# Kernel optimization log

Hardware: AMD Instinct MI355X
Metric: run time of the kernel (lower is better)

Reference implementation:

```python
import jax, jax.numpy as jnp
import numpy as np

B, IN, L0, L1, H, NT = 4096, 1024, 2048, 1024, 128, 512
T = 0.1          # temperature (nonzero -> soft indicator)
EPS = 1e-5       # BatchNorm eps


def setup_inputs() -> dict:
    key = jax.random.key(0)
    ks = jax.random.split(key, 12)

    def he(k, fin, fout):
        return jax.random.normal(k, (fin, fout), jnp.float32) * (2.0 / fin) ** 0.5

    dec_raw = jax.random.uniform(ks[10], (H, IN), jnp.float32)
    # mimics dec_weight_scaled = rand(h, in) / row_sum
    dec_w = dec_raw / dec_raw.sum(axis=1, keepdims=True)

    return {
        "x": jax.random.normal(ks[0], (B, IN), jnp.float32),
        # uniform noise driving the exponential reparameterized draws
        "u": jax.random.uniform(ks[1], (B, NT, H), jnp.float32, minval=1e-7, maxval=1.0),
        "enc1_w": he(ks[2], IN, L0), "enc1_b": jnp.zeros(L0, jnp.float32),
        "bn1_g": jnp.ones(L0, jnp.float32), "bn1_b": jnp.zeros(L0, jnp.float32),
        "enc2_w": he(ks[3], L0, L1), "enc2_b": jnp.zeros(L1, jnp.float32),
        "bn2_g": jnp.ones(L1, jnp.float32), "bn2_b": jnp.zeros(L1, jnp.float32),
        "enc3_w": he(ks[4], L1, H), "enc3_b": jnp.zeros(H, jnp.float32),
        "bn3_g": jnp.ones(H, jnp.float32), "bn3_b": jnp.zeros(H, jnp.float32),
        "inp_lamb_w": jax.random.normal(ks[5], (H, H), jnp.float32) * (1.0 / H) ** 0.5,
        "inp_lamb_b": jnp.zeros(H, jnp.float32),
        "dec_w": dec_w,
    }


def _bn(x, g, b):
    # BatchNorm1d in training mode: batch statistics, biased variance
    m = x.mean(axis=0)
    v = ((x - m) ** 2).mean(axis=0)
    return g * (x - m) / jnp.sqrt(v + EPS) + b


def reference(x, u, enc1_w, enc1_b, bn1_g, bn1_b, enc2_w, enc2_b, bn2_g, bn2_b,
              enc3_w, enc3_b, bn3_g, bn3_b, inp_lamb_w, inp_lamb_b, dec_w):
    # ---- encoder ----
    h = jax.nn.relu(_bn(x @ enc1_w + enc1_b, bn1_g, bn1_b))
    h = jax.nn.relu(_bn(h @ enc2_w + enc2_b, bn2_g, bn2_b))
    h = jax.nn.relu(_bn(h @ enc3_w + enc3_b, bn3_g, bn3_b))
    lamb = jnp.abs(h @ inp_lamb_w + inp_lamb_b)              # [B,H]

    # ---- decoder matrix normalization ----
    diag = jax.lax.stop_gradient(jnp.abs(dec_w.sum(axis=1)))  # [H], detached
    decode = jnp.abs(dec_w) / diag[:, None]                   # [H,IN]
    rate = jnp.clip(lamb * diag, 1e-10, 1e7)                  # [B,H]

    # ---- Poisson rsample via cumulative exponential inter-arrival times ----
    # Exponential(rate) draws: -log(u)/rate ; cumsum over trials; soft indicator
    e = -jnp.log(u) / rate[:, None, :]                        # [B,NT,H]
    times = jnp.cumsum(e, axis=1)                             # [B,NT,H]
    indicator = jax.nn.sigmoid((1.0 - times) / T)             # soft (t != 0)
    samples = indicator.sum(axis=1)                           # [B,H]

    x_rec = samples @ decode                                  # [B,IN]
    return (x_rec, samples, rate, decode)
```

## Files before the change

kernel.cpp:

```cpp
#include <hip/hip_runtime.h>
#include <stdint.h>


typedef __attribute__((ext_vector_type(8))) __bf16 bf16x8;
typedef __attribute__((ext_vector_type(4))) float f32x4;
typedef unsigned short ushort_t;

__device__ __forceinline__ unsigned short f2bf(float f) {
  unsigned int u = __float_as_uint(f);
  unsigned int r = (u + 0x7fffu + ((u >> 16) & 1u)) >> 16;
  return (unsigned short)r;
}
__device__ __forceinline__ float bf2f(unsigned short h) {
  return __uint_as_float(((unsigned int)h) << 16);
}

__device__ __forceinline__ void gll16(const void* g, void* l) {
  __builtin_amdgcn_global_load_lds(
      (const __attribute__((address_space(1))) unsigned int*)g,
      (__attribute__((address_space(3))) unsigned int*)l, 16, 0, 0);
}

__global__ void kconvert_split4(const float4* __restrict__ in, ushort4* __restrict__ hi,
                                ushort4* __restrict__ lo, int n4) {
  int i = blockIdx.x * blockDim.x + threadIdx.x;
  if (i < n4) {
    float4 v = in[i];
    ushort4 h, l;
    h.x = f2bf(v.x); l.x = f2bf(v.x - bf2f(h.x));
    h.y = f2bf(v.y); l.y = f2bf(v.y - bf2f(h.y));
    h.z = f2bf(v.z); l.z = f2bf(v.z - bf2f(h.z));
    h.w = f2bf(v.w); l.w = f2bf(v.w - bf2f(h.w));
    hi[i] = h; lo[i] = l;
  }
}

__global__ void ktranspose_split(const float* __restrict__ in, unsigned short* __restrict__ ohi,
                                 unsigned short* __restrict__ olo, int R, int C) {
  __shared__ unsigned short th[32][33];
  __shared__ unsigned short tl[32][33];
  int c0 = blockIdx.x * 32, r0 = blockIdx.y * 32;
  int tx = threadIdx.x & 31, ty = threadIdx.x >> 5;
#pragma unroll
  for (int i = 0; i < 32; i += 8) {
    float v = in[(size_t)(r0 + ty + i) * C + c0 + tx];
    unsigned short h = f2bf(v);
    th[ty + i][tx] = h;
    tl[ty + i][tx] = f2bf(v - bf2f(h));
  }
  __syncthreads();
#pragma unroll
  for (int i = 0; i < 32; i += 8) {
    ohi[(size_t)(c0 + ty + i) * R + r0 + tx] = th[tx][ty + i];
    olo[(size_t)(c0 + ty + i) * R + r0 + tx] = tl[tx][ty + i];
  }
}

__global__ __launch_bounds__(256) void kgemm3p(
    const unsigned short* __restrict__ Ah, const unsigned short* __restrict__ Al,
    const unsigned short* __restrict__ Bh, const unsigned short* __restrict__ Bl,
    const float* __restrict__ bias, float* __restrict__ C, int N, int K, int kLen,
    float* __restrict__ bnps, float* __restrict__ bnpq, const float* __restrict__ diag) {
  __shared__ unsigned short As[2][4096];
  __shared__ unsigned short Bs[2][4096];
  __shared__ float sred[2][2][128];
  int tid = threadIdx.x;
  int lane = tid & 63;
  int wave = tid >> 6;
  int wm = wave >> 1, wn = wave & 1;
  int rowBase = blockIdx.x * 128;
  int colBase = blockIdx.y * 128;
  int kOff = blockIdx.z * kLen;
  C += (size_t)blockIdx.z * gridDim.x * 128 * N;

  f32x4 acc[4][4];
#pragma unroll
  for (int i = 0; i < 4; i++)
#pragma unroll
    for (int j = 0; j < 4; j++) acc[i][j] = (f32x4){0.f, 0.f, 0.f, 0.f};

  int r4 = tid >> 2;
  int kc = (tid & 3) * 8;
  int lr = lane & 15;
  int lk = (lane >> 4) * 8;

  const unsigned short* Ah0 = Ah + (size_t)(rowBase + r4) * K + kOff + kc;
  const unsigned short* Al0 = Al + (size_t)(rowBase + r4) * K + kOff + kc;
  const unsigned short* Bh0 = Bh + (size_t)(colBase + r4) * K + kOff + kc;
  const unsigned short* Bl0 = Bl + (size_t)(colBase + r4) * K + kOff + kc;
  size_t rstep = (size_t)64 * K;
  char* AsD = (char*)As + tid * 16;
  char* BsD = (char*)Bs + tid * 16;

  gll16(Ah0, AsD);        gll16(Ah0 + rstep, AsD + 4096);
  gll16(Al0, AsD + 8192); gll16(Al0 + rstep, AsD + 12288);
  gll16(Bh0, BsD);        gll16(Bh0 + rstep, BsD + 4096);
  gll16(Bl0, BsD + 8192); gll16(Bl0 + rstep, BsD + 12288);
  __syncthreads();

  int nk = kLen >> 5;
  for (int kt = 0; kt < nk; ++kt) {
    bf16x8 ah[4], al[4], bh[4], bl[4];
#pragma unroll
    for (int mi = 0; mi < 4; mi++) {
      ah[mi] = *(const bf16x8*)&As[0][(wm * 64 + mi * 16 + lr) * 32 + lk];
      al[mi] = *(const bf16x8*)&As[1][(wm * 64 + mi * 16 + lr) * 32 + lk];
      bh[mi] = *(const bf16x8*)&Bs[0][(wn * 64 + mi * 16 + lr) * 32 + lk];
      bl[mi] = *(const bf16x8*)&Bs[1][(wn * 64 + mi * 16 + lr) * 32 + lk];
    }
    __syncthreads();

    if (kt + 1 < nk) {
      int k0 = (kt + 1) << 5;
      gll16(Ah0 + k0, AsD);        gll16(Ah0 + k0 + rstep, AsD + 4096);
      gll16(Al0 + k0, AsD + 8192); gll16(Al0 + k0 + rstep, AsD + 12288);
      gll16(Bh0 + k0, BsD);        gll16(Bh0 + k0 + rstep, BsD + 4096);
      gll16(Bl0 + k0, BsD + 8192); gll16(Bl0 + k0 + rstep, BsD + 12288);
    }

#pragma unroll
    for (int mi = 0; mi < 4; mi++)
#pragma unroll
      for (int ni = 0; ni < 4; ni++) {
        acc[mi][ni] = __builtin_amdgcn_mfma_f32_16x16x32_bf16(ah[mi], bh[ni], acc[mi][ni], 0, 0, 0);
        acc[mi][ni] = __builtin_amdgcn_mfma_f32_16x16x32_bf16(ah[mi], bl[ni], acc[mi][ni], 0, 0, 0);
        acc[mi][ni] = __builtin_amdgcn_mfma_f32_16x16x32_bf16(al[mi], bh[ni], acc[mi][ni], 0, 0, 0);
      }
    __syncthreads();
  }

  int lg = lane >> 4;
  if (diag) {
#pragma unroll
    for (int mi = 0; mi < 4; mi++)
#pragma unroll
      for (int ni = 0; ni < 4; ni++) {
        int col = colBase + wn * 64 + ni * 16 + lr;
        float bv = bias ? bias[col] : 0.0f;
        float dg = diag[col];
#pragma unroll
        for (int j = 0; j < 4; j++) {
          int row = rowBase + wm * 64 + mi * 16 + lg * 4 + j;
          float r = fabsf(acc[mi][ni][j] + bv) * dg;
          C[(size_t)row * N + col] = fminf(fmaxf(r, 1e-10f), 1e7f);
        }
      }
  } else {
    float s[4] = {0.f, 0.f, 0.f, 0.f}, q[4] = {0.f, 0.f, 0.f, 0.f};
#pragma unroll
    for (int mi = 0; mi < 4; mi++)
#pragma unroll
      for (int ni = 0; ni < 4; ni++) {
        int col = colBase + wn * 64 + ni * 16 + lr;
        float bv = bias ? bias[col] : 0.0f;
#pragma unroll
        for (int j = 0; j < 4; j++) {
          int row = rowBase + wm * 64 + mi * 16 + lg * 4 + j;
          float v = acc[mi][ni][j] + bv;
          C[(size_t)row * N + col] = v;
          s[ni] += v;
          q[ni] += v * v;
        }
      }
    if (bnps) {
#pragma unroll
      for (int ni = 0; ni < 4; ni++) {
        s[ni] += __shfl_xor(s[ni], 16); s[ni] += __shfl_xor(s[ni], 32);
        q[ni] += __shfl_xor(q[ni], 16); q[ni] += __shfl_xor(q[ni], 32);
      }
      if (lg == 0) {
#pragma unroll
        for (int ni = 0; ni < 4; ni++) {
          sred[wm][0][wn * 64 + ni * 16 + lr] = s[ni];
          sred[wm][1][wn * 64 + ni * 16 + lr] = q[ni];
        }
      }
      __syncthreads();
      if (tid < 128) {
        bnps[(size_t)blockIdx.x * N + colBase + tid] = sred[0][0][tid] + sred[1][0][tid];
        bnpq[(size_t)blockIdx.x * N + colBase + tid] = sred[0][1][tid] + sred[1][1][tid];
      }
    }
  }
}

__global__ __launch_bounds__(256) void kgemm(
    const unsigned short* __restrict__ A, const unsigned short* __restrict__ BT,
    float* __restrict__ C, int N, int K) {
  __shared__ unsigned short As[4096];
  __shared__ unsigned short Bs[4096];
  int tid = threadIdx.x;
  int lane = tid & 63;
  int wave = tid >> 6;
  int wm = wave >> 1, wn = wave & 1;
  int rowBase = blockIdx.x * 128;
  int colBase = blockIdx.y * 128;

  f32x4 acc[4][4];
#pragma unroll
  for (int i = 0; i < 4; i++)
#pragma unroll
    for (int j = 0; j < 4; j++) acc[i][j] = (f32x4){0.f, 0.f, 0.f, 0.f};

  int r4 = tid >> 2;
  int kc = (tid & 3) * 8;
  int lr = lane & 15;
  int lk = (lane >> 4) * 8;

  const unsigned short* A0 = A + (size_t)(rowBase + r4) * K + kc;
  const unsigned short* B0 = BT + (size_t)(colBase + r4) * K + kc;
  size_t rstep = (size_t)64 * K;
  char* AsD = (char*)As + tid * 16;
  char* BsD = (char*)Bs + tid * 16;

  gll16(A0, AsD); gll16(A0 + rstep, AsD + 4096);
  gll16(B0, BsD); gll16(B0 + rstep, BsD + 4096);
  __syncthreads();

  int nk = K >> 5;
  for (int kt = 0; kt < nk; ++kt) {
    bf16x8 af[4], bfr[4];
#pragma unroll
    for (int mi = 0; mi < 4; mi++) {
      af[mi] = *(const bf16x8*)&As[(wm * 64 + mi * 16 + lr) * 32 + lk];
      bfr[mi] = *(const bf16x8*)&Bs[(wn * 64 + mi * 16 + lr) * 32 + lk];
    }
    __syncthreads();
    if (kt + 1 < nk) {
      int k0 = (kt + 1) << 5;
      gll16(A0 + k0, AsD); gll16(A0 + k0 + rstep, AsD + 4096);
      gll16(B0 + k0, BsD); gll16(B0 + k0 + rstep, BsD + 4096);
    }
#pragma unroll
    for (int mi = 0; mi < 4; mi++)
#pragma unroll
      for (int ni = 0; ni < 4; ni++)
        acc[mi][ni] = __builtin_amdgcn_mfma_f32_16x16x32_bf16(af[mi], bfr[ni], acc[mi][ni], 0, 0, 0);
    __syncthreads();
  }

  int lg = lane >> 4;
#pragma unroll
  for (int mi = 0; mi < 4; mi++)
#pragma unroll
    for (int ni = 0; ni < 4; ni++) {
      int col = colBase + wn * 64 + ni * 16 + lr;
#pragma unroll
      for (int j = 0; j < 4; j++) {
        int row = rowBase + wm * 64 + mi * 16 + lg * 4 + j;
        C[(size_t)row * N + col] = acc[mi][ni][j];
      }
    }
}

__global__ void kbn_partial(const float* __restrict__ y, float* __restrict__ ps,
                            float* __restrict__ pq, int N) {
  int c = blockIdx.x * blockDim.x + threadIdx.x;
  int r0 = blockIdx.y * 128;
  float s = 0.f, q = 0.f;
  for (int r = r0; r < r0 + 128; ++r) {
    float v = y[(size_t)r * N + c];
    s += v;
    q += v * v;
  }
  ps[blockIdx.y * N + c] = s;
  pq[blockIdx.y * N + c] = q;
}

__global__ void kbn_final(const float* __restrict__ ps, const float* __restrict__ pq,
                          const float* __restrict__ g, const float* __restrict__ b,
                          float* __restrict__ scale, float* __restrict__ shift, int N,
                          int stripes) {
  int c = blockIdx.x * blockDim.x + threadIdx.x;
  if (c >= N) return;
  float s = 0.f, q = 0.f;
  for (int i = 0; i < stripes; ++i) {
    s += ps[i * N + c];
    q += pq[i * N + c];
  }
  float m = s * (1.0f / 4096.0f);
  float var = q * (1.0f / 4096.0f) - m * m;
  float sc = g[c] * rsqrtf(var + 1e-5f);
  scale[c] = sc;
  shift[c] = b[c] - m * sc;
}

__global__ void kbn_apply_split4(const float4* __restrict__ y, const float* __restrict__ scale,
                                 const float* __restrict__ shift, ushort4* __restrict__ hhi,
                                 ushort4* __restrict__ hlo, int mask) {
  int i = blockIdx.x * blockDim.x + threadIdx.x;
  int c0 = (i << 2) & mask;
  float4 v = y[i];
  ushort4 h, l;
  float t;
  t = v.x * scale[c0] + shift[c0];         t = t > 0.f ? t : 0.f; h.x = f2bf(t); l.x = f2bf(t - bf2f(h.x));
  t = v.y * scale[c0 + 1] + shift[c0 + 1]; t = t > 0.f ? t : 0.f; h.y = f2bf(t); l.y = f2bf(t - bf2f(h.y));
  t = v.z * scale[c0 + 2] + shift[c0 + 2]; t = t > 0.f ? t : 0.f; h.z = f2bf(t); l.z = f2bf(t - bf2f(h.z));
  t = v.w * scale[c0 + 3] + shift[c0 + 3]; t = t > 0.f ? t : 0.f; h.w = f2bf(t); l.w = f2bf(t - bf2f(h.w));
  hhi[i] = h;
  hlo[i] = l;
}

__global__ void kcombine(const float4* __restrict__ Cp, const float* __restrict__ bias,
                         float4* __restrict__ y, int n4, int splitStride4, int splits, int mask) {
  int i = blockIdx.x * blockDim.x + threadIdx.x;
  if (i >= n4) return;
  int c0 = (i << 2) & mask;
  float4 a = Cp[i];
  for (int z = 1; z < splits; ++z) {
    float4 b = Cp[(size_t)z * splitStride4 + i];
    a.x += b.x; a.y += b.y; a.z += b.z; a.w += b.w;
  }
  a.x += bias[c0]; a.y += bias[c0 + 1]; a.z += bias[c0 + 2]; a.w += bias[c0 + 3];
  y[i] = a;
}

__global__ void kdec(const float* __restrict__ dec_w, float* __restrict__ decode,
                     unsigned short* __restrict__ decT, float* __restrict__ diag) {
  int h = blockIdx.x, tx = threadIdx.x;
  __shared__ float red[256];
  float s = 0.f;
  for (int i = tx; i < 1024; i += 256) s += dec_w[h * 1024 + i];
  red[tx] = s;
  __syncthreads();
  for (int k = 128; k > 0; k >>= 1) {
    if (tx < k) red[tx] += red[tx + k];
    __syncthreads();
  }
  float d = fabsf(red[0]);
  if (tx == 0) diag[h] = d;
  float inv = 1.0f / d;
  for (int i = tx; i < 1024; i += 256) {
    float v = fabsf(dec_w[h * 1024 + i]) * inv;
    decode[h * 1024 + i] = v;
    decT[i * 128 + h] = f2bf(v);
  }
}

__global__ __launch_bounds__(256) void kpoisson(const float* __restrict__ u,
                                                const float* __restrict__ rate,
                                                float* __restrict__ samples,
                                                unsigned short* __restrict__ sb) {
  int tid = blockIdx.x * 256 + threadIdx.x;
  int h = tid & 127;
  int b = tid >> 7;
  float r = rate[tid];
  float inv = 1.0f / r;
  const float* up = u + (size_t)b * (512 * 128) + h;
  float t = 0.f, s = 0.f;
  for (int nt = 0; nt < 512; ++nt) {
    float uv = up[(size_t)nt * 128];
    t += (-__logf(uv)) * inv;
    float z = (t - 1.0f) * 10.0f;
    s += __frcp_rn(1.0f + __expf(z));
    if (t > 4.0f) break;
  }
  samples[tid] = s;
  sb[tid] = f2bf(s);
}

extern "C" void kernel_launch(void* const* d_in, const int* in_sizes, int n_in,
                              void* d_out, int out_size, void* d_ws, size_t ws_size,
                              hipStream_t stream) {
  const float* x = (const float*)d_in[0];
  const float* u = (const float*)d_in[1];
  const float* w1 = (const float*)d_in[2];
  const float* b1 = (const float*)d_in[3];
  const float* g1 = (const float*)d_in[4];
  const float* bb1 = (const float*)d_in[5];
  const float* w2 = (const float*)d_in[6];
  const float* b2 = (const float*)d_in[7];
  const float* g2 = (const float*)d_in[8];
  const float* bb2 = (const float*)d_in[9];
  const float* w3 = (const float*)d_in[10];
  const float* b3 = (const float*)d_in[11];
  const float* g3 = (const float*)d_in[12];
  const float* bb3 = (const float*)d_in[13];
  const float* w4 = (const float*)d_in[14];
  const float* b4 = (const float*)d_in[15];
  const float* dw = (const float*)d_in[16];

  float* out = (float*)d_out;
  float* out_xrec = out;
  float* out_samp = out + 4194304;
  float* out_rate = out + 4718592;
  float* out_dec = out + 5242880;

  char* w = (char*)d_ws;
  unsigned short* xhi = (unsigned short*)w;  w += 8388608;
  unsigned short* xlo = (unsigned short*)w;  w += 8388608;
  unsigned short* w1th = (unsigned short*)w; w += 4194304;
  unsigned short* w1tl = (unsigned short*)w; w += 4194304;
  unsigned short* w2th = (unsigned short*)w; w += 4194304;
  unsigned short* w2tl = (unsigned short*)w; w += 4194304;
  unsigned short* w3th = (unsigned short*)w; w += 262144;
  unsigned short* w3tl = (unsigned short*)w; w += 262144;
  unsigned short* w4th = (unsigned short*)w; w += 32768;
  unsigned short* w4tl = (unsigned short*)w; w += 32768;
  float* y = (float*)w;             w += 33554432;
  unsigned short* h1h = (unsigned short*)w; w += 16777216;
  unsigned short* h1l = (unsigned short*)w; w += 16777216;
  unsigned short* h2h = (unsigned short*)w; w += 8388608;
  unsigned short* h2l = (unsigned short*)w; w += 8388608;
  unsigned short* h3h = (unsigned short*)w; w += 1048576;
  unsigned short* h3l = (unsigned short*)w; w += 1048576;
  float* y3 = (float*)w;            w += 2097152;
  float* Cp = (float*)w;            w += 8388608;
  unsigned short* sb = (unsigned short*)w; w += 1048576;
  unsigned short* dct = (unsigned short*)w; w += 262144;
  float* diag = (float*)w;          w += 1024;
  float* ps = (float*)w;            w += 262144;
  float* pq = (float*)w;            w += 262144;
  float* scale = (float*)w;         w += 8192;
  float* shift = (float*)w;         w += 8192;

  kconvert_split4<<<4096, 256, 0, stream>>>((const float4*)x, (ushort4*)xhi, (ushort4*)xlo, 1048576);
  ktranspose_split<<<dim3(64, 32), 256, 0, stream>>>(w1, w1th, w1tl, 1024, 2048);
  ktranspose_split<<<dim3(32, 64), 256, 0, stream>>>(w2, w2th, w2tl, 2048, 1024);
  ktranspose_split<<<dim3(4, 32), 256, 0, stream>>>(w3, w3th, w3tl, 1024, 128);
  ktranspose_split<<<dim3(4, 4), 256, 0, stream>>>(w4, w4th, w4tl, 128, 128);
  kdec<<<128, 256, 0, stream>>>(dw, out_dec, dct, diag);

  kgemm3p<<<dim3(32, 16), 256, 0, stream>>>(xhi, xlo, w1th, w1tl, b1, y, 2048, 1024, 1024,
                                            ps, pq, nullptr);
  kbn_final<<<8, 256, 0, stream>>>(ps, pq, g1, bb1, scale, shift, 2048, 32);
  kbn_apply_split4<<<8192, 256, 0, stream>>>((const float4*)y, scale, shift, (ushort4*)h1h,
                                             (ushort4*)h1l, 2047);

  kgemm3p<<<dim3(32, 8), 256, 0, stream>>>(h1h, h1l, w2th, w2tl, b2, y, 1024, 2048, 2048,
                                           ps, pq, nullptr);
  kbn_final<<<4, 256, 0, stream>>>(ps, pq, g2, bb2, scale, shift, 1024, 32);
  kbn_apply_split4<<<4096, 256, 0, stream>>>((const float4*)y, scale, shift, (ushort4*)h2h,
                                             (ushort4*)h2l, 1023);

  kgemm3p<<<dim3(32, 1, 4), 256, 0, stream>>>(h2h, h2l, w3th, w3tl, nullptr, Cp, 128, 1024, 256,
                                              nullptr, nullptr, nullptr);
  kcombine<<<512, 256, 0, stream>>>((const float4*)Cp, b3, (float4*)y3, 131072, 131072, 4, 127);
  kbn_partial<<<dim3(1, 32), 128, 0, stream>>>(y3, ps, pq, 128);
  kbn_final<<<1, 128, 0, stream>>>(ps, pq, g3, bb3, scale, shift, 128, 32);
  kbn_apply_split4<<<512, 256, 0, stream>>>((const float4*)y3, scale, shift, (ushort4*)h3h,
                                            (ushort4*)h3l, 127);

  kgemm3p<<<dim3(32, 1), 256, 0, stream>>>(h3h, h3l, w4th, w4tl, b4, out_rate, 128, 128, 128,
                                           nullptr, nullptr, diag);

  kpoisson<<<2048, 256, 0, stream>>>(u, out_rate, out_samp, sb);

  kgemm<<<dim3(32, 8), 256, 0, stream>>>(sb, dct, out_xrec, 1024, 128);
}
```

Baseline: 275.0 us.

## Add 256-row GEMM tile, split-K layer 2, fuse combine with BN stats

Adds a 256x128 tiled three-pass bf16 GEMM kernel used for the first two encoder layers, doubling A-tile reuse of B fragments per block. Layer 2 now uses split-K by 2 into a larger partial buffer, and a new kernel sums the splits, adds bias and computes BatchNorm partial sums in one pass. Layer 3 goes to split-K by 8 with the same fused combine/stats, replacing a separate combine and partial-stat kernel. The cost is more register pressure and fewer blocks per GEMM, plus extra partial-buffer traffic for the split-K layers.

```diff
diff --git a/kernel.cpp b/kernel.cpp
--- a/kernel.cpp
+++ b/kernel.cpp
@@ -4,7 +4,6 @@
 
 typedef __attribute__((ext_vector_type(8))) __bf16 bf16x8;
 typedef __attribute__((ext_vector_type(4))) float f32x4;
-typedef unsigned short ushort_t;
 
 __device__ __forceinline__ unsigned short f2bf(float f) {
   unsigned int u = __float_as_uint(f);
@@ -56,14 +55,137 @@
   }
 }
 
+__global__ __launch_bounds__(256, 2) void kgemm3p256(
+    const unsigned short* __restrict__ Ah, const unsigned short* __restrict__ Al,
+    const unsigned short* __restrict__ Bh, const unsigned short* __restrict__ Bl,
+    const float* __restrict__ bias, float* __restrict__ C, int N, int K, int kLen,
+    float* __restrict__ bnps, float* __restrict__ bnpq) {
+  __shared__ unsigned short As[2][8192];
+  __shared__ unsigned short Bs[2][4096];
+  __shared__ float sred[2][2][128];
+  int tid = threadIdx.x;
+  int lane = tid & 63;
+  int wave = tid >> 6;
+  int wm = wave >> 1, wn = wave & 1;
+  int rowBase = blockIdx.x * 256;
+  int colBase = blockIdx.y * 128;
+  int kOff = blockIdx.z * kLen;
+  C += (size_t)blockIdx.z * gridDim.x * 256 * N;
+
+  f32x4 acc[8][4];
+#pragma unroll
+  for (int i = 0; i < 8; i++)
+#pragma unroll
+    for (int j = 0; j < 4; j++) acc[i][j] = (f32x4){0.f, 0.f, 0.f, 0.f};
+
+  int r4 = tid >> 2;
+  int kc = (tid & 3) * 8;
+  int lr = lane & 15;
+  int lk = (lane >> 4) * 8;
+
+  const unsigned short* Ah0 = Ah + (size_t)(rowBase + r4) * K + kOff + kc;
+  const unsigned short* Al0 = Al + (size_t)(rowBase + r4) * K + kOff + kc;
+  const unsigned short* Bh0 = Bh + (size_t)(colBase + r4) * K + kOff + kc;
+  const unsigned short* Bl0 = Bl + (size_t)(colBase + r4) * K + kOff + kc;
+  size_t rstep = (size_t)64 * K;
+  char* AsD = (char*)As + tid * 16;
+  char* BsD = (char*)Bs + tid * 16;
+
+  auto STAGE = [&](int k0) {
+    gll16(Ah0 + k0, AsD);
+    gll16(Ah0 + k0 + rstep, AsD + 4096);
+    gll16(Ah0 + k0 + 2 * rstep, AsD + 8192);
+    gll16(Ah0 + k0 + 3 * rstep, AsD + 12288);
+    gll16(Al0 + k0, AsD + 16384);
+    gll16(Al0 + k0 + rstep, AsD + 20480);
+    gll16(Al0 + k0 + 2 * rstep, AsD + 24576);
+    gll16(Al0 + k0 + 3 * rstep, AsD + 28672);
+    gll16(Bh0 + k0, BsD);
+    gll16(Bh0 + k0 + rstep, BsD + 4096);
+    gll16(Bl0 + k0, BsD + 8192);
+    gll16(Bl0 + k0 + rstep, BsD + 12288);
+  };
+
+  STAGE(0);
+  __syncthreads();
+
+  int nk = kLen >> 5;
+  for (int kt = 0; kt < nk; ++kt) {
+    bf16x8 ah[8], al[8], bh[4], bl[4];
+#pragma unroll
+    for (int mi = 0; mi < 8; mi++) {
+      ah[mi] = *(const bf16x8*)&As[0][(wm * 128 + mi * 16 + lr) * 32 + lk];
+      al[mi] = *(const bf16x8*)&As[1][(wm * 128 + mi * 16 + lr) * 32 + lk];
+    }
+#pragma unroll
+    for (int ni = 0; ni < 4; ni++) {
+      bh[ni] = *(const bf16x8*)&Bs[0][(wn * 64 + ni * 16 + lr) * 32 + lk];
+      bl[ni] = *(const bf16x8*)&Bs[1][(wn * 64 + ni * 16 + lr) * 32 + lk];
+    }
+    __syncthreads();
+
+    if (kt + 1 < nk) STAGE((kt + 1) << 5);
+
+#pragma unroll
+    for (int mi = 0; mi < 8; mi++)
+#pragma unroll
+      for (int ni = 0; ni < 4; ni++) {
+        acc[mi][ni] = __builtin_amdgcn_mfma_f32_16x16x32_bf16(ah[mi], bh[ni], acc[mi][ni], 0, 0, 0);
+        acc[mi][ni] = __builtin_amdgcn_mfma_f32_16x16x32_bf16(ah[mi], bl[ni], acc[mi][ni], 0, 0, 0);
+      }
+#pragma unroll
+    for (int mi = 0; mi < 8; mi++)
+#pragma unroll
+      for (int ni = 0; ni < 4; ni++)
+        acc[mi][ni] = __builtin_amdgcn_mfma_f32_16x16x32_bf16(al[mi], bh[ni], acc[mi][ni], 0, 0, 0);
+    __syncthreads();
+  }
+
+  int lg = lane >> 4;
+  float s[4] = {0.f, 0.f, 0.f, 0.f}, q[4] = {0.f, 0.f, 0.f, 0.f};
+#pragma unroll
+  for (int mi = 0; mi < 8; mi++)
+#pragma unroll
+    for (int ni = 0; ni < 4; ni++) {
+      int col = colBase + wn * 64 + ni * 16 + lr;
+      float bv = bias ? bias[col] : 0.0f;
+#pragma unroll
+      for (int j = 0; j < 4; j++) {
+        int row = rowBase + wm * 128 + mi * 16 + lg * 4 + j;
+        float v = acc[mi][ni][j] + bv;
+        C[(size_t)row * N + col] = v;
+        s[ni] += v;
+        q[ni] += v * v;
+      }
+    }
+  if (bnps) {
+#pragma unroll
+    for (int ni = 0; ni < 4; ni++) {
+      s[ni] += __shfl_xor(s[ni], 16); s[ni] += __shfl_xor(s[ni], 32);
+      q[ni] += __shfl_xor(q[ni], 16); q[ni] += __shfl_xor(q[ni], 32);
+    }
+    if (lg == 0) {
+#pragma unroll
+      for (int ni = 0; ni < 4; ni++) {
+        sred[wm][0][wn * 64 + ni * 16 + lr] = s[ni];
+        sred[wm][1][wn * 64 + ni * 16 + lr] = q[ni];
+      }
+    }
+    __syncthreads();
+    if (tid < 128) {
+      bnps[(size_t)blockIdx.x * N + colBase + tid] = sred[0][0][tid] + sred[1][0][tid];
+      bnpq[(size_t)blockIdx.x * N + colBase + tid] = sred[0][1][tid] + sred[1][1][tid];
+    }
+  }
+}
+
 __global__ __launch_bounds__(256) void kgemm3p(
     const unsigned short* __restrict__ Ah, const unsigned short* __restrict__ Al,
     const unsigned short* __restrict__ Bh, const unsigned short* __restrict__ Bl,
     const float* __restrict__ bias, float* __restrict__ C, int N, int K, int kLen,
-    float* __restrict__ bnps, float* __restrict__ bnpq, const float* __restrict__ diag) {
+    const float* __restrict__ diag) {
   __shared__ unsigned short As[2][4096];
   __shared__ unsigned short Bs[2][4096];
-  __shared__ float sred[2][2][128];
   int tid = threadIdx.x;
   int lane = tid & 63;
   int wave = tid >> 6;
@@ -109,7 +231,6 @@
       bl[mi] = *(const bf16x8*)&Bs[1][(wn * 64 + mi * 16 + lr) * 32 + lk];
     }
     __syncthreads();
-
     if (kt + 1 < nk) {
       int k0 = (kt + 1) << 5;
       gll16(Ah0 + k0, AsD);        gll16(Ah0 + k0 + rstep, AsD + 4096);
@@ -117,7 +238,6 @@
       gll16(Bh0 + k0, BsD);        gll16(Bh0 + k0 + rstep, BsD + 4096);
       gll16(Bl0 + k0, BsD + 8192); gll16(Bl0 + k0 + rstep, BsD + 12288);
     }
-
 #pragma unroll
     for (int mi = 0; mi < 4; mi++)
 #pragma unroll
@@ -130,58 +250,21 @@
   }
 
   int lg = lane >> 4;
-  if (diag) {
-#pragma unroll
-    for (int mi = 0; mi < 4; mi++)
-#pragma unroll
-      for (int ni = 0; ni < 4; ni++) {
-        int col = colBase + wn * 64 + ni * 16 + lr;
-        float bv = bias ? bias[col] : 0.0f;
-        float dg = diag[col];
-#pragma unroll
-        for (int j = 0; j < 4; j++) {
-          int row = rowBase + wm * 64 + mi * 16 + lg * 4 + j;
-          float r = fabsf(acc[mi][ni][j] + bv) * dg;
-          C[(size_t)row * N + col] = fminf(fmaxf(r, 1e-10f), 1e7f);
-        }
+#pragma unroll
+  for (int mi = 0; mi < 4; mi++)
+#pragma unroll
+    for (int ni = 0; ni < 4; ni++) {
+      int col = colBase + wn * 64 + ni * 16 + lr;
+      float bv = bias ? bias[col] : 0.0f;
+      float dg = diag ? diag[col] : 0.0f;
+#pragma unroll
+      for (int j = 0; j < 4; j++) {
+        int row = rowBase + wm * 64 + mi * 16 + lg * 4 + j;
+        float v = acc[mi][ni][j] + bv;
+        if (diag) v = fminf(fmaxf(fabsf(v) * dg, 1e-10f), 1e7f);
+        C[(size_t)row * N + col] = v;
       }
-  } else {
-    float s[4] = {0.f, 0.f, 0.f, 0.f}, q[4] = {0.f, 0.f, 0.f, 0.f};
-#pragma unroll
-    for (int mi = 0; mi < 4; mi++)
-#pragma unroll
-      for (int ni = 0; ni < 4; ni++) {
-        int col = colBase + wn * 64 + ni * 16 + lr;
-        float bv = bias ? bias[col] : 0.0f;
-#pragma unroll
-        for (int j = 0; j < 4; j++) {
-          int row = rowBase + wm * 64 + mi * 16 + lg * 4 + j;
-          float v = acc[mi][ni][j] + bv;
-          C[(size_t)row * N + col] = v;
-          s[ni] += v;
-          q[ni] += v * v;
-        }
-      }
-    if (bnps) {
-#pragma unroll
-      for (int ni = 0; ni < 4; ni++) {
-        s[ni] += __shfl_xor(s[ni], 16); s[ni] += __shfl_xor(s[ni], 32);
-        q[ni] += __shfl_xor(q[ni], 16); q[ni] += __shfl_xor(q[ni], 32);
-      }
-      if (lg == 0) {
-#pragma unroll
-        for (int ni = 0; ni < 4; ni++) {
-          sred[wm][0][wn * 64 + ni * 16 + lr] = s[ni];
-          sred[wm][1][wn * 64 + ni * 16 + lr] = q[ni];
-        }
-      }
-      __syncthreads();
-      if (tid < 128) {
-        bnps[(size_t)blockIdx.x * N + colBase + tid] = sred[0][0][tid] + sred[1][0][tid];
-        bnpq[(size_t)blockIdx.x * N + colBase + tid] = sred[0][1][tid] + sred[1][1][tid];
-      }
-    }
-  }
+    }
 }
 
 __global__ __launch_bounds__(256) void kgemm(
@@ -253,13 +336,17 @@
     }
 }
 
-__global__ void kbn_partial(const float* __restrict__ y, float* __restrict__ ps,
-                            float* __restrict__ pq, int N) {
-  int c = blockIdx.x * blockDim.x + threadIdx.x;
+__global__ void kcombine_bn(const float* __restrict__ Cp, const float* __restrict__ bias,
+                            float* __restrict__ y, float* __restrict__ ps, float* __restrict__ pq,
+                            int N, int splits, int splitStride) {
+  int c = blockIdx.x * 128 + threadIdx.x;
   int r0 = blockIdx.y * 128;
+  float bv = bias[c];
   float s = 0.f, q = 0.f;
   for (int r = r0; r < r0 + 128; ++r) {
-    float v = y[(size_t)r * N + c];
+    float v = bv;
+    for (int z = 0; z < splits; ++z) v += Cp[(size_t)z * splitStride + (size_t)r * N + c];
+    y[(size_t)r * N + c] = v;
     s += v;
     q += v * v;
   }
@@ -299,20 +386,6 @@
   t = v.w * scale[c0 + 3] + shift[c0 + 3]; t = t > 0.f ? t : 0.f; h.w = f2bf(t); l.w = f2bf(t - bf2f(h.w));
   hhi[i] = h;
   hlo[i] = l;
-}
-
-__global__ void kcombine(const float4* __restrict__ Cp, const float* __restrict__ bias,
-                         float4* __restrict__ y, int n4, int splitStride4, int splits, int mask) {
-  int i = blockIdx.x * blockDim.x + threadIdx.x;
-  if (i >= n4) return;
-  int c0 = (i << 2) & mask;
-  float4 a = Cp[i];
-  for (int z = 1; z < splits; ++z) {
-    float4 b = Cp[(size_t)z * splitStride4 + i];
-    a.x += b.x; a.y += b.y; a.z += b.z; a.w += b.w;
-  }
-  a.x += bias[c0]; a.y += bias[c0 + 1]; a.z += bias[c0 + 2]; a.w += bias[c0 + 3];
-  y[i] = a;
 }
 
 __global__ void kdec(const float* __restrict__ dec_w, float* __restrict__ decode,
@@ -405,7 +478,7 @@
   unsigned short* h3h = (unsigned short*)w; w += 1048576;
   unsigned short* h3l = (unsigned short*)w; w += 1048576;
   float* y3 = (float*)w;            w += 2097152;
-  float* Cp = (float*)w;            w += 8388608;
+  float* Cp = (float*)w;            w += 33554432;
   unsigned short* sb = (unsigned short*)w; w += 1048576;
   unsigned short* dct = (unsigned short*)w; w += 262144;
   float* diag = (float*)w;          w += 1024;
@@ -421,28 +494,28 @@
   ktranspose_split<<<dim3(4, 4), 256, 0, stream>>>(w4, w4th, w4tl, 128, 128);
   kdec<<<128, 256, 0, stream>>>(dw, out_dec, dct, diag);
 
-  kgemm3p<<<dim3(32, 16), 256, 0, stream>>>(xhi, xlo, w1th, w1tl, b1, y, 2048, 1024, 1024,
-                                            ps, pq, nullptr);
-  kbn_final<<<8, 256, 0, stream>>>(ps, pq, g1, bb1, scale, shift, 2048, 32);
+  kgemm3p256<<<dim3(16, 16), 256, 0, stream>>>(xhi, xlo, w1th, w1tl, b1, y, 2048, 1024, 1024,
+                                               ps, pq);
+  kbn_final<<<8, 256, 0, stream>>>(ps, pq, g1, bb1, scale, shift, 2048, 16);
   kbn_apply_split4<<<8192, 256, 0, stream>>>((const float4*)y, scale, shift, (ushort4*)h1h,
                                              (ushort4*)h1l, 2047);
 
-  kgemm3p<<<dim3(32, 8), 256, 0, stream>>>(h1h, h1l, w2th, w2tl, b2, y, 1024, 2048, 2048,
-                                           ps, pq, nullptr);
+  kgemm3p256<<<dim3(16, 8, 2), 256, 0, stream>>>(h1h, h1l, w2th, w2tl, nullptr, Cp, 1024, 2048,
+                                                 1024, nullptr, nullptr);
+  kcombine_bn<<<dim3(8, 32), 128, 0, stream>>>(Cp, b2, y, ps, pq, 1024, 2, 4194304);
   kbn_final<<<4, 256, 0, stream>>>(ps, pq, g2, bb2, scale, shift, 1024, 32);
   kbn_apply_split4<<<4096, 256, 0, stream>>>((const float4*)y, scale, shift, (ushort4*)h2h,
                                              (ushort4*)h2l, 1023);
 
-  kgemm3p<<<dim3(32, 1, 4), 256, 0, stream>>>(h2h, h2l, w3th, w3tl, nullptr, Cp, 128, 1024, 256,
-                                              nullptr, nullptr, nullptr);
-  kcombine<<<512, 256, 0, stream>>>((const float4*)Cp, b3, (float4*)y3, 131072, 131072, 4, 127);
-  kbn_partial<<<dim3(1, 32), 128, 0, stream>>>(y3, ps, pq, 128);
+  kgemm3p<<<dim3(32, 1, 8), 256, 0, stream>>>(h2h, h2l, w3th, w3tl, nullptr, Cp, 128, 1024, 128,
+                                              nullptr);
+  kcombine_bn<<<dim3(1, 32), 128, 0, stream>>>(Cp, b3, y3, ps, pq, 128, 8, 524288);
   kbn_final<<<1, 128, 0, stream>>>(ps, pq, g3, bb3, scale, shift, 128, 32);
   kbn_apply_split4<<<512, 256, 0, stream>>>((const float4*)y3, scale, shift, (ushort4*)h3h,
                                             (ushort4*)h3l, 127);
 
   kgemm3p<<<dim3(32, 1), 256, 0, stream>>>(h3h, h3l, w4th, w4tl, b4, out_rate, 128, 128, 128,
-                                           nullptr, nullptr, diag);
+                                           diag);
 
   kpoisson<<<2048, 256, 0, stream>>>(u, out_rate, out_samp, sb);
 
```

New measurement: 599.6 us. 2.18x slower.

## Split-K the second and third encoder GEMMs and fuse combine with BN stats

Applied to the files above, without the earlier changes.

The second encoder GEMM moves from a 256-block launch to split-K over 2 slices (512 blocks) writing partial sums. A new kernel sums the partials, adds the bias and accumulates BatchNorm partial statistics in the same pass. The third GEMM goes from 4 to 8 K-splits, and the separate combine and bn_partial kernels are merged. This trades extra global traffic for the fp32 partial buffers (a larger Cp workspace) against better occupancy on the many-CU GPU, and the column-per-thread combine loop is scalar and strided by row.

```diff
diff --git a/kernel.cpp b/kernel.cpp
--- a/kernel.cpp
+++ b/kernel.cpp
@@ -4,7 +4,6 @@
 
 typedef __attribute__((ext_vector_type(8))) __bf16 bf16x8;
 typedef __attribute__((ext_vector_type(4))) float f32x4;
-typedef unsigned short ushort_t;
 
 __device__ __forceinline__ unsigned short f2bf(float f) {
   unsigned int u = __float_as_uint(f);
@@ -253,13 +252,17 @@
     }
 }
 
-__global__ void kbn_partial(const float* __restrict__ y, float* __restrict__ ps,
-                            float* __restrict__ pq, int N) {
-  int c = blockIdx.x * blockDim.x + threadIdx.x;
+__global__ void kcombine_bn(const float* __restrict__ Cp, const float* __restrict__ bias,
+                            float* __restrict__ y, float* __restrict__ ps, float* __restrict__ pq,
+                            int N, int splits, int splitStride) {
+  int c = blockIdx.x * 128 + threadIdx.x;
   int r0 = blockIdx.y * 128;
+  float bv = bias[c];
   float s = 0.f, q = 0.f;
   for (int r = r0; r < r0 + 128; ++r) {
-    float v = y[(size_t)r * N + c];
+    float v = bv;
+    for (int z = 0; z < splits; ++z) v += Cp[(size_t)z * splitStride + (size_t)r * N + c];
+    y[(size_t)r * N + c] = v;
     s += v;
     q += v * v;
   }
@@ -299,20 +302,6 @@
   t = v.w * scale[c0 + 3] + shift[c0 + 3]; t = t > 0.f ? t : 0.f; h.w = f2bf(t); l.w = f2bf(t - bf2f(h.w));
   hhi[i] = h;
   hlo[i] = l;
-}
-
-__global__ void kcombine(const float4* __restrict__ Cp, const float* __restrict__ bias,
-                         float4* __restrict__ y, int n4, int splitStride4, int splits, int mask) {
-  int i = blockIdx.x * blockDim.x + threadIdx.x;
-  if (i >= n4) return;
-  int c0 = (i << 2) & mask;
-  float4 a = Cp[i];
-  for (int z = 1; z < splits; ++z) {
-    float4 b = Cp[(size_t)z * splitStride4 + i];
-    a.x += b.x; a.y += b.y; a.z += b.z; a.w += b.w;
-  }
-  a.x += bias[c0]; a.y += bias[c0 + 1]; a.z += bias[c0 + 2]; a.w += bias[c0 + 3];
-  y[i] = a;
 }
 
 __global__ void kdec(const float* __restrict__ dec_w, float* __restrict__ decode,
@@ -405,7 +394,7 @@
   unsigned short* h3h = (unsigned short*)w; w += 1048576;
   unsigned short* h3l = (unsigned short*)w; w += 1048576;
   float* y3 = (float*)w;            w += 2097152;
-  float* Cp = (float*)w;            w += 8388608;
+  float* Cp = (float*)w;            w += 33554432;
   unsigned short* sb = (unsigned short*)w; w += 1048576;
   unsigned short* dct = (unsigned short*)w; w += 262144;
   float* diag = (float*)w;          w += 1024;
@@ -427,16 +416,16 @@
   kbn_apply_split4<<<8192, 256, 0, stream>>>((const float4*)y, scale, shift, (ushort4*)h1h,
                                              (ushort4*)h1l, 2047);
 
-  kgemm3p<<<dim3(32, 8), 256, 0, stream>>>(h1h, h1l, w2th, w2tl, b2, y, 1024, 2048, 2048,
-                                           ps, pq, nullptr);
+  kgemm3p<<<dim3(32, 8, 2), 256, 0, stream>>>(h1h, h1l, w2th, w2tl, nullptr, Cp, 1024, 2048,
+                                              1024, nullptr, nullptr, nullptr);
+  kcombine_bn<<<dim3(8, 32), 128, 0, stream>>>(Cp, b2, y, ps, pq, 1024, 2, 4194304);
   kbn_final<<<4, 256, 0, stream>>>(ps, pq, g2, bb2, scale, shift, 1024, 32);
   kbn_apply_split4<<<4096, 256, 0, stream>>>((const float4*)y, scale, shift, (ushort4*)h2h,
                                              (ushort4*)h2l, 1023);
 
-  kgemm3p<<<dim3(32, 1, 4), 256, 0, stream>>>(h2h, h2l, w3th, w3tl, nullptr, Cp, 128, 1024, 256,
+  kgemm3p<<<dim3(32, 1, 8), 256, 0, stream>>>(h2h, h2l, w3th, w3tl, nullptr, Cp, 128, 1024, 128,
                                               nullptr, nullptr, nullptr);
-  kcombine<<<512, 256, 0, stream>>>((const float4*)Cp, b3, (float4*)y3, 131072, 131072, 4, 127);
-  kbn_partial<<<dim3(1, 32), 128, 0, stream>>>(y3, ps, pq, 128);
+  kcombine_bn<<<dim3(1, 32), 128, 0, stream>>>(Cp, b3, y3, ps, pq, 128, 8, 524288);
   kbn_final<<<1, 128, 0, stream>>>(ps, pq, g3, bb3, scale, shift, 128, 32);
   kbn_apply_split4<<<512, 256, 0, stream>>>((const float4*)y3, scale, shift, (ushort4*)h3h,
                                             (ushort4*)h3l, 127);
```

Result: slower. 558.1 us (+102.9%).
